# Optimization experiments

Measured on AMD Instinct MI355X. Metric: run time of the kernel, lower is better.

## Reference

```python
import jax, jax.numpy as jnp
import numpy as np
import math

MODEL_DIM = 2048
NUM_EXPERTS = 64
N_TOKENS = 16384
CAPACITY_FACTOR = 1.0
MIN_CAPACITY = 8
THRESHOLD = 0.5


def _threshold_gating(logits):
    # Faithful jax translation of main_thresholdGating (training path, threshold>0).
    # Note: the torch code truncates sorted columns to the data-dependent
    # explore_top_k_num; we keep the full E columns instead. This is exactly
    # equivalent: dropped columns are all-unchosen (importance 0), and using
    # arange(E,0,-1) instead of arange(K,0,-1) shifts every chosen importance
    # by the same constant (E-K), which preserves the per-expert top-k order.
    N, E = logits.shape
    capacity = max(int(math.ceil(N / E * CAPACITY_FACTOR)), MIN_CAPACITY)  # static

    gates = jax.nn.softmax(logits, axis=1)                    # [N,E]
    indices1 = jnp.argmax(gates, axis=1)                      # top-1 expert per token
    mask1 = jax.nn.one_hot(indices1, E, dtype=gates.dtype)    # [N,E]

    # sorted gates + cumsum threshold selection
    gates_sorted, gates_idx = jax.lax.top_k(gates, E)         # [N,E] descending
    cum = jnp.cumsum(gates_sorted, axis=-1)
    chosen = (cum - gates_sorted) < THRESHOLD                 # [N,E] bool
    chosen = chosen.at[:, 0].set(True)                        # always keep top-1

    # scatter importance = rank-priority + gate prob into expert columns
    rank_imp = jnp.arange(E, 0, -1, dtype=gates.dtype)[None, :] + gates_sorted
    imp = jnp.where(chosen, rank_imp, jnp.zeros_like(rank_imp))
    row = jnp.arange(N)[:, None]
    # gates_idx rows are permutations of experts -> no scatter collisions
    tam = jnp.zeros((N, E), gates.dtype).at[row, gates_idx].set(imp)  # [N,E]

    # capacity truncation: per expert column keep the `capacity` tokens with
    # highest importance
    top_idx = jax.lax.top_k(tam.T, capacity)[1]               # [E, capacity]
    keep = jnp.zeros((N, E), gates.dtype).at[top_idx, jnp.arange(E)[:, None]].set(1.0)
    final_mask = ((tam * keep) > 0).astype(gates.dtype)       # [N,E]

    combine_weights = gates * final_mask

    # load-balancing aux loss (GShard style)
    me = jnp.mean(gates, axis=0)
    ce = jnp.mean(mask1, axis=0)
    l_aux = jnp.sum(me * ce) * E
    return l_aux, combine_weights


def setup_inputs() -> dict:
    key = jax.random.key(0)
    kx, kw = jax.random.split(key)
    x = jax.random.normal(kx, (N_TOKENS, MODEL_DIM), dtype=jnp.float32)
    # gate weight of wg = Linear(model_dim, num_experts, bias=False)
    W = jax.random.normal(kw, (NUM_EXPERTS, MODEL_DIM), dtype=jnp.float32) / math.sqrt(MODEL_DIM)
    return {"x": x, "W": W}


def reference(x, W):
    logits = x @ W.T                                          # [N,E]
    l_aux, combine_weights = _threshold_gating(logits)
    return l_aux, combine_weights
```

## Files before the change

kernel.cpp:

```cpp
#include <hip/hip_runtime.h>
#include <cstdint>
#include <cstddef>

#define N_TOK  16384
#define NEXP   64
#define KDIM   2048
#define CAP    256
#define NE_TOT ((size_t)N_TOK * NEXP)

typedef __attribute__((ext_vector_type(8))) short short8;
typedef __attribute__((ext_vector_type(4))) float f32x4;

__device__ __forceinline__ unsigned short bf16_rtn(float f) {
  unsigned u = __float_as_uint(f);
  u += 0x7FFFu + ((u >> 16) & 1u);
  return (unsigned short)(u >> 16);
}
__device__ __forceinline__ float bf16_f(unsigned short h) {
  return __uint_as_float((unsigned)h << 16);
}
__device__ __forceinline__ f32x4 MF(short8 a, short8 b, f32x4 c) {
  return __builtin_amdgcn_mfma_f32_16x16x32_bf16(a, b, c, 0, 0, 0);
}

__global__ __launch_bounds__(256) void wdigits(const float* __restrict__ W,
    unsigned short* __restrict__ Wh, unsigned short* __restrict__ Wl,
    unsigned short* __restrict__ Wq) {
  const int e = (int)blockIdx.x * 256 + (int)threadIdx.x;
  const int col = e >> 11;
  const int k   = e & 2047;
  const float w = W[(size_t)col * KDIM + k];
  const unsigned short h = bf16_rtn(w);
  const float r1 = w - bf16_f(h);
  const unsigned short lo = bf16_rtn(r1);
  const float r2 = r1 - bf16_f(lo);
  const unsigned short q = bf16_rtn(r2);
  const size_t idx = (size_t)(k >> 3) * 512 + (size_t)col * 8 + (k & 7);
  Wh[idx] = h; Wl[idx] = lo; Wq[idx] = q;
}

__device__ __forceinline__ void cvt8(float4 a, float4 b,
                                     short8& h, short8& lo, short8& q) {
  float f[8] = {a.x, a.y, a.z, a.w, b.x, b.y, b.z, b.w};
#pragma unroll
  for (int j = 0; j < 8; ++j) {
    unsigned short hh = bf16_rtn(f[j]);
    float r1 = f[j] - bf16_f(hh);
    unsigned short ll = bf16_rtn(r1);
    float r2 = r1 - bf16_f(ll);
    h[j] = (short)hh; lo[j] = (short)ll; q[j] = (short)bf16_rtn(r2);
  }
}

template <int KS>
__global__ __launch_bounds__(256, 4) void gemm_mfma(const float* __restrict__ x,
    const unsigned short* __restrict__ Wh, const unsigned short* __restrict__ Wl,
    const unsigned short* __restrict__ Wq, float* __restrict__ part) {
  constexpr int NSTEP = (KDIM / KS) / 32;
  const int tid = (int)threadIdx.x;
  const int l   = tid & 63;
  const int wv  = tid >> 6;
  const int ks  = (int)blockIdx.x >> 7;
  const int mt  = (((int)blockIdx.x & 127) << 2) + wv;
  const int row0 = mt * 32;
  const int kBeg = ks * (KDIM / KS);
  const int lr = l & 15;
  const int lk = l >> 4;

  f32x4 acc00 = {0.f,0.f,0.f,0.f}, acc01 = {0.f,0.f,0.f,0.f};
  f32x4 acc02 = {0.f,0.f,0.f,0.f}, acc03 = {0.f,0.f,0.f,0.f};
  f32x4 acc10 = {0.f,0.f,0.f,0.f}, acc11 = {0.f,0.f,0.f,0.f};
  f32x4 acc12 = {0.f,0.f,0.f,0.f}, acc13 = {0.f,0.f,0.f,0.f};

  const float* pa0 = x + (size_t)(row0 + lr) * KDIM + kBeg + lk * 8;
  const float* pa1 = pa0 + (size_t)16 * KDIM;
  const size_t bbase = ((size_t)((kBeg >> 3) + lk)) * 64 + lr;
  const short8* BH = (const short8*)Wh + bbase;
  const short8* BL = (const short8*)Wl + bbase;
  const short8* BQ = (const short8*)Wq + bbase;

  float4 A0a = *(const float4*)pa0;
  float4 A0b = *(const float4*)(pa0 + 4);
  float4 A1a = *(const float4*)pa1;
  float4 A1b = *(const float4*)(pa1 + 4);
  short8 bh = BH[0], bl = BL[0], bq = BQ[0];

  for (int s = 0; s < NSTEP; ++s) {
    const int so = s * 256;
    short8 a_h0, a_l0, a_q0, a_h1, a_l1, a_q1;
    cvt8(A0a, A0b, a_h0, a_l0, a_q0);
    cvt8(A1a, A1b, a_h1, a_l1, a_q1);
    if (s + 1 < NSTEP) {
      pa0 += 32; pa1 += 32;
      A0a = *(const float4*)pa0;
      A0b = *(const float4*)(pa0 + 4);
      A1a = *(const float4*)pa1;
      A1b = *(const float4*)(pa1 + 4);
    }

#define CT_BLOCK(ACC0, ACC1)                                         \
    ACC0 = MF(a_h0, bh, ACC0); ACC0 = MF(a_h0, bl, ACC0);            \
    ACC0 = MF(a_l0, bh, ACC0); ACC0 = MF(a_l0, bl, ACC0);            \
    ACC0 = MF(a_q0, bh, ACC0); ACC0 = MF(a_h0, bq, ACC0);            \
    ACC1 = MF(a_h1, bh, ACC1); ACC1 = MF(a_h1, bl, ACC1);            \
    ACC1 = MF(a_l1, bh, ACC1); ACC1 = MF(a_l1, bl, ACC1);            \
    ACC1 = MF(a_q1, bh, ACC1); ACC1 = MF(a_h1, bq, ACC1);

    short8 nh = BH[so + 16], nl = BL[so + 16], nq = BQ[so + 16];
    CT_BLOCK(acc00, acc10)
    bh = nh; bl = nl; bq = nq;
    nh = BH[so + 32]; nl = BL[so + 32]; nq = BQ[so + 32];
    CT_BLOCK(acc01, acc11)
    bh = nh; bl = nl; bq = nq;
    nh = BH[so + 48]; nl = BL[so + 48]; nq = BQ[so + 48];
    CT_BLOCK(acc02, acc12)
    bh = nh; bl = nl; bq = nq;
    const int ni = (s + 1 < NSTEP) ? so + 256 : so;
    nh = BH[ni]; nl = BL[ni]; nq = BQ[ni];
    CT_BLOCK(acc03, acc13)
    bh = nh; bl = nl; bq = nq;
#undef CT_BLOCK
  }

  float* pout = part + (size_t)ks * NE_TOT;
  const int rb = row0 + lk * 4;
#pragma unroll
  for (int r = 0; r < 4; ++r) {
    pout[(size_t)(rb + r) * 64 +  0 + lr] = acc00[r];
    pout[(size_t)(rb + r) * 64 + 16 + lr] = acc01[r];
    pout[(size_t)(rb + r) * 64 + 32 + lr] = acc02[r];
    pout[(size_t)(rb + r) * 64 + 48 + lr] = acc03[r];
    pout[(size_t)(rb + 16 + r) * 64 +  0 + lr] = acc10[r];
    pout[(size_t)(rb + 16 + r) * 64 + 16 + lr] = acc11[r];
    pout[(size_t)(rb + 16 + r) * 64 + 32 + lr] = acc12[r];
    pout[(size_t)(rb + 16 + r) * 64 + 48 + lr] = acc13[r];
  }
}

template <int KS>
__global__ __launch_bounds__(1024) void gate_rows(const float* __restrict__ part,
                                                  float* __restrict__ gatesT,
                                                  float* __restrict__ tamT) {
  __shared__ float gt[64][65];
  __shared__ float tt[64][65];
  const int tid  = (int)threadIdx.x;
  const int lane = tid & 63;
  const int wid  = tid >> 6;
  const int row0 = (int)blockIdx.x * 64;

#pragma unroll
  for (int r = 0; r < 4; ++r) {
    const int rloc = wid * 4 + r;
    const size_t base = (size_t)(row0 + rloc) * NEXP;

    float logit = 0.f;
#pragma unroll
    for (int s = 0; s < KS; ++s)
      logit += part[(size_t)s * NE_TOT + base + lane];

    float m = logit;
#pragma unroll
    for (int off = 32; off > 0; off >>= 1) m = fmaxf(m, __shfl_xor(m, off));
    float p = expf(logit - m);
    float sum = p;
#pragma unroll
    for (int off = 32; off > 0; off >>= 1) sum += __shfl_xor(sum, off);
    const float gate = p / sum;

    float g = gate;
    int idx = lane;
#pragma unroll
    for (int k = 2; k <= 64; k <<= 1) {
#pragma unroll
      for (int j = k >> 1; j > 0; j >>= 1) {
        float og = __shfl_xor(g, j);
        int   oi = __shfl_xor(idx, j);
        bool iLower     = (lane & j) == 0;
        bool wantFirst  = ((lane & k) == 0) ? iLower : !iLower;
        bool otherFirst = (og > g) || (og == g && oi < idx);
        if (otherFirst == wantFirst) { g = og; idx = oi; }
      }
    }

    float cum = g;
#pragma unroll
    for (int off = 1; off < 64; off <<= 1) {
      float t = __shfl_up(cum, off);
      if (lane >= off) cum += t;
    }
    const bool chosen = (lane == 0) || ((cum - g) < 0.5f);
    const float imp = chosen ? ((float)(NEXP - lane) + g) : 0.f;

    gt[rloc][lane] = gate;
    tt[rloc][idx]  = imp;
  }
  __syncthreads();

#pragma unroll
  for (int p = 0; p < 4; ++p) {
    const int e = p * 16 + wid;
    gatesT[(size_t)e * N_TOK + row0 + lane] = gt[lane][e];
    tamT  [(size_t)e * N_TOK + row0 + lane] = tt[lane][e];
  }
}

__global__ __launch_bounds__(1024) void expert_select(
    const float* __restrict__ gatesT, const float* __restrict__ tamT,
    float* __restrict__ me_sum, int* __restrict__ ce_cnt,
    float* __restrict__ combT) {
  __shared__ int   hist16[16][256];
  __shared__ int   hist[256];
  __shared__ float wsum[16];
  __shared__ int   wice[16];
  __shared__ int   wnnz[16];
  __shared__ int   wcnt[16];
  __shared__ unsigned sh_prefix;
  __shared__ int      sh_k;
  __shared__ int      sh_nnz;

  const int e    = (int)blockIdx.x;
  const int tid  = (int)threadIdx.x;
  const int lane = tid & 63;
  const int wid  = tid >> 6;
  const float* tcol = tamT   + (size_t)e * N_TOK;
  const float* gcol = gatesT + (size_t)e * N_TOK;

  float gsum = 0.f;
  int ccnt = 0, nnzl = 0;
#pragma unroll
  for (int k = 0; k < 4; ++k) {
    int i4 = tid + k * 1024;
    float4 tv = reinterpret_cast<const float4*>(tcol)[i4];
    float4 gv = reinterpret_cast<const float4*>(gcol)[i4];
    gsum += gv.x + gv.y + gv.z + gv.w;
    ccnt += (tv.x > 64.f) + (tv.y > 64.f) + (tv.z > 64.f) + (tv.w > 64.f);
    nnzl += (tv.x != 0.f) + (tv.y != 0.f) + (tv.z != 0.f) + (tv.w != 0.f);
  }
#pragma unroll
  for (int off = 32; off > 0; off >>= 1) {
    gsum += __shfl_xor(gsum, off);
    ccnt += __shfl_xor(ccnt, off);
    nnzl += __shfl_xor(nnzl, off);
  }
  if (lane == 0) { wsum[wid] = gsum; wice[wid] = ccnt; wnnz[wid] = nnzl; }
  __syncthreads();
  if (tid == 0) {
    float t = 0.f; int c = 0, nz = 0;
    for (int w = 0; w < 16; ++w) { t += wsum[w]; c += wice[w]; nz += wnnz[w]; }
    me_sum[e] = t; ce_cnt[e] = c; sh_nnz = nz;
  }
  __syncthreads();
  const int nnz = sh_nnz;

  unsigned vstar = 0u;
  int meq = 0;
  if (nnz > CAP) {
    unsigned prefix = 0;
    int krem = CAP;
    for (int round = 0; round < 4; ++round) {
      const int shift = 24 - 8 * round;
      const unsigned maskAbove =
          (round == 0) ? 0u : (0xFFFFFFFFu << (shift + 8));
      for (int z = tid; z < 16 * 256; z += 1024) ((int*)hist16)[z] = 0;
      __syncthreads();
#pragma unroll
      for (int k = 0; k < 16; ++k) {
        unsigned u = __float_as_uint(tcol[tid + k * 1024]);
        if (u != 0u && (u & maskAbove) == prefix)
          atomicAdd(&hist16[wid][(u >> shift) & 255], 1);
      }
      __syncthreads();
      if (tid < 256) {
        int s = 0;
#pragma unroll
        for (int w = 0; w < 16; ++w) s += hist16[w][tid];
        hist[tid] = s;
      }
      __syncthreads();
      if (wid == 0) {
        int h0 = hist[lane * 4 + 0], h1 = hist[lane * 4 + 1];
        int h2 = hist[lane * 4 + 2], h3 = hist[lane * 4 + 3];
        int lsum = h0 + h1 + h2 + h3;
        int suf = lsum;
#pragma unroll
        for (int off = 1; off < 64; off <<= 1) {
          int t = __shfl_down(suf, off);
          if (lane + off < 64) suf += t;
        }
        int above = suf - lsum;
        int S3 = above + h3, S2 = S3 + h2, S1 = S2 + h1, S0 = S1 + h0;
        if (S0 >= krem && S1    < krem) { sh_prefix = prefix | ((unsigned)(lane*4+0) << shift); sh_k = krem - S1;    }
        if (S1 >= krem && S2    < krem) { sh_prefix = prefix | ((unsigned)(lane*4+1) << shift); sh_k = krem - S2;    }
        if (S2 >= krem && S3    < krem) { sh_prefix = prefix | ((unsigned)(lane*4+2) << shift); sh_k = krem - S3;    }
        if (S3 >= krem && above < krem) { sh_prefix = prefix | ((unsigned)(lane*4+3) << shift); sh_k = krem - above; }
      }
      __syncthreads();
      prefix = sh_prefix;
      krem   = sh_k;
      __syncthreads();
    }
    vstar = prefix;
    meq   = krem;
  }

  float4 tq[4];
#pragma unroll
  for (int q = 0; q < 4; ++q)
    tq[q] = reinterpret_cast<const float4*>(tcol)[tid * 4 + q];
  int cnt = 0;
#pragma unroll
  for (int q = 0; q < 4; ++q) {
    cnt += (__float_as_uint(tq[q].x) == vstar);
    cnt += (__float_as_uint(tq[q].y) == vstar);
    cnt += (__float_as_uint(tq[q].z) == vstar);
    cnt += (__float_as_uint(tq[q].w) == vstar);
  }
  int inc = cnt;
#pragma unroll
  for (int off = 1; off < 64; off <<= 1) {
    int t = __shfl_up(inc, off);
    if (lane >= off) inc += t;
  }
  if (lane == 63) wcnt[wid] = inc;
  __syncthreads();
  if (tid == 0) {
    int run = 0;
    for (int w = 0; w < 16; ++w) { int t = wcnt[w]; wcnt[w] = run; run += t; }
  }
  __syncthreads();
  int exc = (inc - cnt) + wcnt[wid];

  float* ccol = combT + (size_t)e * N_TOK;
#pragma unroll
  for (int q = 0; q < 4; ++q) {
    float4 gq = reinterpret_cast<const float4*>(gcol)[tid * 4 + q];
    float ov[4];
    const float tv[4] = {tq[q].x, tq[q].y, tq[q].z, tq[q].w};
    const float gv[4] = {gq.x, gq.y, gq.z, gq.w};
#pragma unroll
    for (int j = 0; j < 4; ++j) {
      unsigned u = __float_as_uint(tv[j]);
      bool keep;
      if (u == vstar) { keep = (exc < meq); ++exc; }
      else            { keep = (u > vstar); }
      ov[j] = (keep && u != 0u) ? gv[j] : 0.f;
    }
    reinterpret_cast<float4*>(ccol)[tid * 4 + q] =
        make_float4(ov[0], ov[1], ov[2], ov[3]);
  }
}

__global__ __launch_bounds__(1024) void transpose_out(
    const float* __restrict__ combT, float* __restrict__ out1,
    const float* __restrict__ me_sum, const int* __restrict__ ce_cnt,
    float* __restrict__ out0) {
  __shared__ float tile[64][65];
  const int tid  = (int)threadIdx.x;
  const int lane = tid & 63;
  const int wid  = tid >> 6;
  const int tok0 = (int)blockIdx.x * 64;
#pragma unroll
  for (int p = 0; p < 4; ++p) {
    const int e = p * 16 + wid;
    tile[lane][e] = combT[(size_t)e * N_TOK + tok0 + lane];
  }
  __syncthreads();
#pragma unroll
  for (int q = 0; q < 4; ++q) {
    const int tok = q * 16 + wid;
    out1[(size_t)(tok0 + tok) * NEXP + lane] = tile[tok][lane];
  }
  if (blockIdx.x == 0 && wid == 0) {
    float v = (me_sum[lane] / (float)N_TOK) *
              ((float)ce_cnt[lane] / (float)N_TOK);
#pragma unroll
    for (int off = 32; off > 0; off >>= 1) v += __shfl_xor(v, off);
    if (lane == 0) out0[0] = v * (float)NEXP;
  }
}

extern "C" void kernel_launch(void* const* d_in, const int* in_sizes, int n_in,
                              void* d_out, int out_size, void* d_ws, size_t ws_size,
                              hipStream_t stream) {
  const float* x = (const float*)d_in[0];
  const float* W = (const float*)d_in[1];
  float* out = (float*)d_out;
  float* ws  = (float*)d_ws;

  const bool ks8 = ws_size >= (size_t)(8 + 2) * NE_TOT * 4 + 1024;
  const int  KS  = ks8 ? 8 : 4;

  float* part   = ws;
  float* combT  = ws;
  float* gatesT = ws + (size_t)KS * NE_TOT;
  float* tamT   = gatesT + NE_TOT;
  float* me     = tamT + NE_TOT;
  int*   ce     = (int*)(me + 64);

  unsigned short* Wh = (unsigned short*)gatesT;
  unsigned short* Wl = Wh + (size_t)NEXP * KDIM;
  unsigned short* Wq = Wl + (size_t)NEXP * KDIM;

  wdigits<<<(NEXP * KDIM) / 256, 256, 0, stream>>>(W, Wh, Wl, Wq);
  if (ks8) gemm_mfma<8><<<128 * 8, 256, 0, stream>>>(x, Wh, Wl, Wq, part);
  else     gemm_mfma<4><<<128 * 4, 256, 0, stream>>>(x, Wh, Wl, Wq, part);
  if (ks8) gate_rows<8><<<N_TOK / 64, 1024, 0, stream>>>(part, gatesT, tamT);
  else     gate_rows<4><<<N_TOK / 64, 1024, 0, stream>>>(part, gatesT, tamT);
  expert_select<<<NEXP, 1024, 0, stream>>>(gatesT, tamT, me, ce, combT);
  transpose_out<<<N_TOK / 64, 1024, 0, stream>>>(combT, out + 1, me, ce, out);
}
```

Baseline: 81.67 us.

## Use packed bf16 conversion and halve per-wave row tile in split-K GEMM

Replaces the scalar three-way bf16 digit split of x with the packed v_cvt_pk_bf16_f32 instruction, cutting the VALU work that feeds the MFMAs. Each wave now covers 16 rows instead of 32, so the grid doubles and register pressure drops; the launch-bounds occupancy hint is removed. The cost is that each B (weight digit) fragment is reused across half as many rows, so weight loads per FLOP double. The A prefetch is also reordered so the next loads are issued before the conversion.

```diff
diff --git a/kernel.cpp b/kernel.cpp
--- a/kernel.cpp
+++ b/kernel.cpp
@@ -10,6 +10,7 @@
 
 typedef __attribute__((ext_vector_type(8))) short short8;
 typedef __attribute__((ext_vector_type(4))) float f32x4;
+typedef __attribute__((ext_vector_type(4))) unsigned int uint4x;
 
 __device__ __forceinline__ unsigned short bf16_rtn(float f) {
   unsigned u = __float_as_uint(f);
@@ -21,6 +22,17 @@
 }
 __device__ __forceinline__ f32x4 MF(short8 a, short8 b, f32x4 c) {
   return __builtin_amdgcn_mfma_f32_16x16x32_bf16(a, b, c, 0, 0, 0);
+}
+__device__ __forceinline__ unsigned cvt_pk(float a, float b) {
+  unsigned r;
+  asm("v_cvt_pk_bf16_f32 %0, %1, %2" : "=v"(r) : "v"(a), "v"(b));
+  return r;
+}
+__device__ __forceinline__ float lo16f(unsigned u) {
+  return __uint_as_float(u << 16);
+}
+__device__ __forceinline__ float hi16f(unsigned u) {
+  return __uint_as_float(u & 0xFFFF0000u);
 }
 
 __global__ __launch_bounds__(256) void wdigits(const float* __restrict__ W,
@@ -39,101 +51,100 @@
   Wh[idx] = h; Wl[idx] = lo; Wq[idx] = q;
 }
 
-__device__ __forceinline__ void cvt8(float4 a, float4 b,
-                                     short8& h, short8& lo, short8& q) {
-  float f[8] = {a.x, a.y, a.z, a.w, b.x, b.y, b.z, b.w};
-#pragma unroll
-  for (int j = 0; j < 8; ++j) {
-    unsigned short hh = bf16_rtn(f[j]);
-    float r1 = f[j] - bf16_f(hh);
-    unsigned short ll = bf16_rtn(r1);
-    float r2 = r1 - bf16_f(ll);
-    h[j] = (short)hh; lo[j] = (short)ll; q[j] = (short)bf16_rtn(r2);
-  }
+__device__ __forceinline__ void cvt8pk(float4 a, float4 b,
+                                       short8& h, short8& lo, short8& q) {
+  const float f0 = a.x, f1 = a.y, f2 = a.z, f3 = a.w;
+  const float f4 = b.x, f5 = b.y, f6 = b.z, f7 = b.w;
+  const unsigned h0 = cvt_pk(f0, f1), h1 = cvt_pk(f2, f3);
+  const unsigned h2 = cvt_pk(f4, f5), h3 = cvt_pk(f6, f7);
+  const float r0 = f0 - lo16f(h0), r1 = f1 - hi16f(h0);
+  const float r2 = f2 - lo16f(h1), r3 = f3 - hi16f(h1);
+  const float r4 = f4 - lo16f(h2), r5 = f5 - hi16f(h2);
+  const float r6 = f6 - lo16f(h3), r7 = f7 - hi16f(h3);
+  const unsigned l0 = cvt_pk(r0, r1), l1 = cvt_pk(r2, r3);
+  const unsigned l2 = cvt_pk(r4, r5), l3 = cvt_pk(r6, r7);
+  const float s0 = r0 - lo16f(l0), s1 = r1 - hi16f(l0);
+  const float s2 = r2 - lo16f(l1), s3 = r3 - hi16f(l1);
+  const float s4 = r4 - lo16f(l2), s5 = r5 - hi16f(l2);
+  const float s6 = r6 - lo16f(l3), s7 = r7 - hi16f(l3);
+  const unsigned q0 = cvt_pk(s0, s1), q1 = cvt_pk(s2, s3);
+  const unsigned q2 = cvt_pk(s4, s5), q3 = cvt_pk(s6, s7);
+  h  = __builtin_bit_cast(short8, (uint4x){h0, h1, h2, h3});
+  lo = __builtin_bit_cast(short8, (uint4x){l0, l1, l2, l3});
+  q  = __builtin_bit_cast(short8, (uint4x){q0, q1, q2, q3});
 }
 
 template <int KS>
-__global__ __launch_bounds__(256, 4) void gemm_mfma(const float* __restrict__ x,
+__global__ __launch_bounds__(256) void gemm_mfma(const float* __restrict__ x,
     const unsigned short* __restrict__ Wh, const unsigned short* __restrict__ Wl,
     const unsigned short* __restrict__ Wq, float* __restrict__ part) {
   constexpr int NSTEP = (KDIM / KS) / 32;
   const int tid = (int)threadIdx.x;
   const int l   = tid & 63;
   const int wv  = tid >> 6;
-  const int ks  = (int)blockIdx.x >> 7;
-  const int mt  = (((int)blockIdx.x & 127) << 2) + wv;
-  const int row0 = mt * 32;
+  const int ks  = (int)blockIdx.x >> 8;
+  const int mt  = (((int)blockIdx.x & 255) << 2) + wv;
+  const int row0 = mt * 16;
   const int kBeg = ks * (KDIM / KS);
   const int lr = l & 15;
   const int lk = l >> 4;
 
-  f32x4 acc00 = {0.f,0.f,0.f,0.f}, acc01 = {0.f,0.f,0.f,0.f};
-  f32x4 acc02 = {0.f,0.f,0.f,0.f}, acc03 = {0.f,0.f,0.f,0.f};
-  f32x4 acc10 = {0.f,0.f,0.f,0.f}, acc11 = {0.f,0.f,0.f,0.f};
-  f32x4 acc12 = {0.f,0.f,0.f,0.f}, acc13 = {0.f,0.f,0.f,0.f};
-
-  const float* pa0 = x + (size_t)(row0 + lr) * KDIM + kBeg + lk * 8;
-  const float* pa1 = pa0 + (size_t)16 * KDIM;
+  f32x4 acc0 = {0.f,0.f,0.f,0.f}, acc1 = {0.f,0.f,0.f,0.f};
+  f32x4 acc2 = {0.f,0.f,0.f,0.f}, acc3 = {0.f,0.f,0.f,0.f};
+
+  const float* pa = x + (size_t)(row0 + lr) * KDIM + kBeg + lk * 8;
   const size_t bbase = ((size_t)((kBeg >> 3) + lk)) * 64 + lr;
   const short8* BH = (const short8*)Wh + bbase;
   const short8* BL = (const short8*)Wl + bbase;
   const short8* BQ = (const short8*)Wq + bbase;
 
-  float4 A0a = *(const float4*)pa0;
-  float4 A0b = *(const float4*)(pa0 + 4);
-  float4 A1a = *(const float4*)pa1;
-  float4 A1b = *(const float4*)(pa1 + 4);
+  float4 A0 = *(const float4*)pa;
+  float4 A1 = *(const float4*)(pa + 4);
   short8 bh = BH[0], bl = BL[0], bq = BQ[0];
 
   for (int s = 0; s < NSTEP; ++s) {
     const int so = s * 256;
-    short8 a_h0, a_l0, a_q0, a_h1, a_l1, a_q1;
-    cvt8(A0a, A0b, a_h0, a_l0, a_q0);
-    cvt8(A1a, A1b, a_h1, a_l1, a_q1);
+    float4 N0, N1;
     if (s + 1 < NSTEP) {
-      pa0 += 32; pa1 += 32;
-      A0a = *(const float4*)pa0;
-      A0b = *(const float4*)(pa0 + 4);
-      A1a = *(const float4*)pa1;
-      A1b = *(const float4*)(pa1 + 4);
+      pa += 32;
+      N0 = *(const float4*)pa;
+      N1 = *(const float4*)(pa + 4);
     }
-
-#define CT_BLOCK(ACC0, ACC1)                                         \
-    ACC0 = MF(a_h0, bh, ACC0); ACC0 = MF(a_h0, bl, ACC0);            \
-    ACC0 = MF(a_l0, bh, ACC0); ACC0 = MF(a_l0, bl, ACC0);            \
-    ACC0 = MF(a_q0, bh, ACC0); ACC0 = MF(a_h0, bq, ACC0);            \
-    ACC1 = MF(a_h1, bh, ACC1); ACC1 = MF(a_h1, bl, ACC1);            \
-    ACC1 = MF(a_l1, bh, ACC1); ACC1 = MF(a_l1, bl, ACC1);            \
-    ACC1 = MF(a_q1, bh, ACC1); ACC1 = MF(a_h1, bq, ACC1);
-
-    short8 nh = BH[so + 16], nl = BL[so + 16], nq = BQ[so + 16];
-    CT_BLOCK(acc00, acc10)
+    short8 a_h, a_l, a_q;
+    cvt8pk(A0, A1, a_h, a_l, a_q);
+
+#define CT_BLOCK(ACC)                                   \
+    ACC = MF(a_h, bh, ACC); ACC = MF(a_h, bl, ACC);     \
+    ACC = MF(a_l, bh, ACC); ACC = MF(a_l, bl, ACC);     \
+    ACC = MF(a_q, bh, ACC); ACC = MF(a_h, bq, ACC);
+
+    short8 nh, nl, nq;
+    nh = BH[so + 16]; nl = BL[so + 16]; nq = BQ[so + 16];
+    CT_BLOCK(acc0)
     bh = nh; bl = nl; bq = nq;
     nh = BH[so + 32]; nl = BL[so + 32]; nq = BQ[so + 32];
-    CT_BLOCK(acc01, acc11)
+    CT_BLOCK(acc1)
     bh = nh; bl = nl; bq = nq;
     nh = BH[so + 48]; nl = BL[so + 48]; nq = BQ[so + 48];
-    CT_BLOCK(acc02, acc12)
+    CT_BLOCK(acc2)
     bh = nh; bl = nl; bq = nq;
     const int ni = (s + 1 < NSTEP) ? so + 256 : so;
     nh = BH[ni]; nl = BL[ni]; nq = BQ[ni];
-    CT_BLOCK(acc03, acc13)
+    CT_BLOCK(acc3)
     bh = nh; bl = nl; bq = nq;
 #undef CT_BLOCK
+
+    if (s + 1 < NSTEP) { A0 = N0; A1 = N1; }
   }
 
   float* pout = part + (size_t)ks * NE_TOT;
   const int rb = row0 + lk * 4;
 #pragma unroll
   for (int r = 0; r < 4; ++r) {
-    pout[(size_t)(rb + r) * 64 +  0 + lr] = acc00[r];
-    pout[(size_t)(rb + r) * 64 + 16 + lr] = acc01[r];
-    pout[(size_t)(rb + r) * 64 + 32 + lr] = acc02[r];
-    pout[(size_t)(rb + r) * 64 + 48 + lr] = acc03[r];
-    pout[(size_t)(rb + 16 + r) * 64 +  0 + lr] = acc10[r];
-    pout[(size_t)(rb + 16 + r) * 64 + 16 + lr] = acc11[r];
-    pout[(size_t)(rb + 16 + r) * 64 + 32 + lr] = acc12[r];
-    pout[(size_t)(rb + 16 + r) * 64 + 48 + lr] = acc13[r];
+    pout[(size_t)(rb + r) * 64 +  0 + lr] = acc0[r];
+    pout[(size_t)(rb + r) * 64 + 16 + lr] = acc1[r];
+    pout[(size_t)(rb + r) * 64 + 32 + lr] = acc2[r];
+    pout[(size_t)(rb + r) * 64 + 48 + lr] = acc3[r];
   }
 }
 
@@ -402,8 +413,8 @@
   unsigned short* Wq = Wl + (size_t)NEXP * KDIM;
 
   wdigits<<<(NEXP * KDIM) / 256, 256, 0, stream>>>(W, Wh, Wl, Wq);
-  if (ks8) gemm_mfma<8><<<128 * 8, 256, 0, stream>>>(x, Wh, Wl, Wq, part);
-  else     gemm_mfma<4><<<128 * 4, 256, 0, stream>>>(x, Wh, Wl, Wq, part);
+  if (ks8) gemm_mfma<8><<<256 * 8, 256, 0, stream>>>(x, Wh, Wl, Wq, part);
+  else     gemm_mfma<4><<<256 * 4, 256, 0, stream>>>(x, Wh, Wl, Wq, part);
   if (ks8) gate_rows<8><<<N_TOK / 64, 1024, 0, stream>>>(part, gatesT, tamT);
   else     gate_rows<4><<<N_TOK / 64, 1024, 0, stream>>>(part, gatesT, tamT);
   expert_select<<<NEXP, 1024, 0, stream>>>(gatesT, tamT, me, ce, combT);
```

Measured after the change: 87.35 us. 7.0% more time.
